# Kernel tuning notes

Measured on AMD Instinct MI355X. Metric: run time of the kernel, lower is better.

## Reference

```python
import jax, jax.numpy as jnp
import numpy as np

B = 65536
IN_DIM = 512
H0, H1 = 256, 128
HEAD_H = 64
D = 12
K_MAX = 3
EPS = 1e-5
# predecessor indices per disease (topologically ordered DAG)
PRED_LISTS = [[], [0], [0], [1, 2], [0, 3], [2], [4, 5], [1, 6], [3, 7], [6, 8], [5, 9], [8, 10, 9]]


def setup_inputs() -> dict:
    key = jax.random.key(0)
    ks = jax.random.split(key, 16)
    x = jax.random.normal(ks[0], (B, IN_DIM), jnp.float32)
    enc_W0 = jax.random.normal(ks[1], (IN_DIM, H0), jnp.float32) * 0.04
    enc_b0 = jnp.zeros((H0,), jnp.float32)
    bn0_g = jnp.ones((H0,), jnp.float32)
    bn0_b = jnp.zeros((H0,), jnp.float32)
    bn0_m = jax.random.normal(ks[2], (H0,), jnp.float32) * 0.1
    bn0_v = jax.random.uniform(ks[3], (H0,), jnp.float32, 0.5, 1.5)
    enc_W1 = jax.random.normal(ks[4], (H0, H1), jnp.float32) * 0.06
    enc_b1 = jnp.zeros((H1,), jnp.float32)
    bn1_g = jnp.ones((H1,), jnp.float32)
    bn1_b = jnp.zeros((H1,), jnp.float32)
    bn1_m = jax.random.normal(ks[5], (H1,), jnp.float32) * 0.1
    bn1_v = jax.random.uniform(ks[6], (H1,), jnp.float32, 0.5, 1.5)
    w_init = jax.random.normal(ks[7], (D, H1), jnp.float32) * 0.09   # head.layer1 (pass-1 logit)
    b_init = jnp.zeros((D,), jnp.float32)
    Wz = jax.random.normal(ks[8], (D, H1, HEAD_H), jnp.float32) * 0.09   # head first layer, z-columns
    Wp = jax.random.normal(ks[9], (D, K_MAX, HEAD_H), jnp.float32) * 0.09  # head first layer, predecessor columns (padded)
    bh = jnp.zeros((D, HEAD_H), jnp.float32)
    Wo = jax.random.normal(ks[10], (D, HEAD_H), jnp.float32) * 0.12
    bo = jnp.zeros((D,), jnp.float32)
    idx = np.zeros((D, K_MAX), np.int32)
    w = np.zeros((D, K_MAX), np.float32)
    for d, preds in enumerate(PRED_LISTS):
        for j, p in enumerate(preds):
            idx[d, j] = p
            w[d, j] = 0.5  # DAG edge weight; zero entries are padding
    return {"x": x, "enc_W0": enc_W0, "enc_b0": enc_b0, "bn0_g": bn0_g, "bn0_b": bn0_b,
            "bn0_m": bn0_m, "bn0_v": bn0_v, "enc_W1": enc_W1, "enc_b1": enc_b1,
            "bn1_g": bn1_g, "bn1_b": bn1_b, "bn1_m": bn1_m, "bn1_v": bn1_v,
            "w_init": w_init, "b_init": b_init, "Wz": Wz, "Wp": Wp, "bh": bh,
            "Wo": Wo, "bo": bo, "pred_w": jnp.asarray(w), "pred_idx": jnp.asarray(idx)}


def reference(x, enc_W0, enc_b0, bn0_g, bn0_b, bn0_m, bn0_v, enc_W1, enc_b1,
              bn1_g, bn1_b, bn1_m, bn1_v, w_init, b_init, Wz, Wp, bh, Wo, bo,
              pred_w, pred_idx):
    # Shared encoder: Linear -> BatchNorm(eval stats) -> ReLU, twice (dropout identity at eval)
    h = x @ enc_W0 + enc_b0
    h = jax.nn.relu((h - bn0_m) * jax.lax.rsqrt(bn0_v + EPS) * bn0_g + bn0_b)
    z = h @ enc_W1 + enc_b1
    z = jax.nn.relu((z - bn1_m) * jax.lax.rsqrt(bn1_v + EPS) * bn1_g + bn1_b)  # [B, H1]
    # Pass 1: initial per-disease prediction = sigmoid(head.layer1(z))
    p = jax.nn.sigmoid(z @ w_init.T + b_init)  # [B, D]
    # Pass 2: DAG gather of predecessor predictions, edge-weighted; padding slots have weight 0
    aug = p[:, pred_idx] * pred_w  # [B, D, K_MAX]
    # Per-disease head: Linear(H1 + k -> HEAD_H) split into z-part + predecessor-part, ReLU, Linear(HEAD_H -> 1), sigmoid
    hid = jax.nn.relu(jnp.einsum('be,deh->bdh', z, Wz) + jnp.einsum('bdk,dkh->bdh', aug, Wp) + bh)
    out = jax.nn.sigmoid(jnp.einsum('bdh,dh->bd', hid, Wo) + bo)  # [B, D] = torch.cat of final_preds
    return out
```

## Files before the change

kernel.cpp:

```cpp
#include <hip/hip_runtime.h>

#define B_TOT   65536
#define IN_DIM  512
#define H0      256
#define H1      128
#define HH      64
#define NDIS    12

typedef __bf16 bf16_t;
typedef __bf16 bf16x4 __attribute__((ext_vector_type(4)));
typedef __bf16 bf16x8 __attribute__((ext_vector_type(8)));
typedef float  f32x4  __attribute__((ext_vector_type(4)));
typedef float  floatx4 __attribute__((ext_vector_type(4)));

#define WS_W0T   0u
#define WS_W1T   262144u
#define WS_WZT   327680u
#define WS_WIT   524288u
#define WS_AL0   528384u
#define WS_BE0   529408u
#define WS_AL1   530432u
#define WS_BE1   530944u
#define WS_NEED  531456u

#define L_XS0    0u
#define L_W0S0   5120u
#define L_XS1    25600u
#define L_W0S1   30720u
#define L_HS     0u
#define L_WZS    0u
#define L_ZS     34816u
#define L_PS     52224u
#define L_WIS    56320u
#define L_TOTAL  60672u

__global__ void prep_kernel(const float* __restrict__ W0, const float* __restrict__ b0,
                            const float* __restrict__ g0, const float* __restrict__ bb0,
                            const float* __restrict__ mm0, const float* __restrict__ vv0,
                            const float* __restrict__ W1, const float* __restrict__ b1,
                            const float* __restrict__ g1, const float* __restrict__ bb1,
                            const float* __restrict__ mm1, const float* __restrict__ vv1,
                            const float* __restrict__ w_init, const float* __restrict__ Wz,
                            char* __restrict__ ws)
{
    bf16_t* W0t = (bf16_t*)(ws + WS_W0T);
    bf16_t* W1t = (bf16_t*)(ws + WS_W1T);
    bf16_t* Wzt = (bf16_t*)(ws + WS_WZT);
    bf16_t* wiT = (bf16_t*)(ws + WS_WIT);
    float* al0 = (float*)(ws + WS_AL0);
    float* be0 = (float*)(ws + WS_BE0);
    float* al1 = (float*)(ws + WS_AL1);
    float* be1 = (float*)(ws + WS_BE1);

    int t = blockIdx.x * 256 + threadIdx.x;

    {
        int c = t >> 9, k = t & 511;
        W0t[t] = (bf16_t)W0[k * H0 + c];
    }
    if (t < H1 * H0) {
        int c = t >> 8, k = t & 255;
        W1t[t] = (bf16_t)W1[k * H1 + c];
    }
    if (t < NDIS * HH * H1) {
        int d = t >> 13, r = t & 8191, h = r >> 7, e = r & 127;
        Wzt[t] = (bf16_t)Wz[d * 8192 + e * 64 + h];
    }
    if (t < 16 * H1) {
        int d = t >> 7, e = t & 127;
        wiT[t] = (d < NDIS) ? (bf16_t)w_init[d * H1 + e] : (bf16_t)0.0f;
    }
    if (t < H0) {
        float a = g0[t] * rsqrtf(vv0[t] + 1e-5f);
        al0[t] = a;
        be0[t] = (b0[t] - mm0[t]) * a + bb0[t];
    }
    if (t < H1) {
        float a = g1[t] * rsqrtf(vv1[t] + 1e-5f);
        al1[t] = a;
        be1[t] = (b1[t] - mm1[t]) * a + bb1[t];
    }
}

__global__ __launch_bounds__(512, 3) void fused_kernel(
    const float* __restrict__ x,
    const bf16_t* __restrict__ W0t, const bf16_t* __restrict__ W1t,
    const float* __restrict__ al0, const float* __restrict__ be0,
    const float* __restrict__ al1, const float* __restrict__ be1,
    const bf16_t* __restrict__ Wzt, const bf16_t* __restrict__ wiT,
    const float* __restrict__ b_init, const float* __restrict__ Wp,
    const float* __restrict__ bh, const float* __restrict__ Wo,
    const float* __restrict__ bo, const float* __restrict__ pred_w,
    const int* __restrict__ pred_idx, float* __restrict__ out)
{
    __shared__ __align__(16) char smem[L_TOTAL];

    const int tid  = threadIdx.x;
    const int lane = tid & 63, wid = tid >> 6;
    const int l15 = lane & 15, lg = lane >> 4;
    const int m0 = blockIdx.x * 64;

    {
        bf16_t* wis = (bf16_t*)(smem + L_WIS);
        if (tid < 256) {
            int row = tid >> 4, k8 = (tid & 15) << 3;
            *(bf16x8*)(wis + row * 136 + k8) = *(const bf16x8*)(wiT + row * H1 + k8);
        }
    }

    const int wr = wid >> 2, wc = wid & 3;
    const int xrow = tid >> 3, xc4 = (tid & 7) << 2;
    const int wrow = tid >> 2, wk8 = (tid & 3) << 3;
    const float*  xp  = x + (m0 + xrow) * IN_DIM + xc4;
    const bf16_t* wp0 = W0t + wrow * IN_DIM + wk8;
    const bf16_t* wp1 = W0t + (wrow + 128) * IN_DIM + wk8;

    bf16_t* xsb[2]  = { (bf16_t*)(smem + L_XS0),  (bf16_t*)(smem + L_XS1)  };
    bf16_t* w0sb[2] = { (bf16_t*)(smem + L_W0S0), (bf16_t*)(smem + L_W0S1) };

    floatx4 xvA, xvB;
    bf16x8  wvA0, wvA1, wvB0, wvB1;

#define LOAD_A(ks) { xvA = *(const floatx4*)(xp + (ks) * 32); \
                     wvA0 = *(const bf16x8*)(wp0 + (ks) * 32); \
                     wvA1 = *(const bf16x8*)(wp1 + (ks) * 32); }
#define LOAD_B(ks) { xvB = *(const floatx4*)(xp + (ks) * 32); \
                     wvB0 = *(const bf16x8*)(wp0 + (ks) * 32); \
                     wvB1 = *(const bf16x8*)(wp1 + (ks) * 32); }
#define STORE_A(bi) { bf16x4 xo; xo[0]=(bf16_t)xvA[0]; xo[1]=(bf16_t)xvA[1]; \
                      xo[2]=(bf16_t)xvA[2]; xo[3]=(bf16_t)xvA[3]; \
                      *(bf16x4*)(xsb[bi] + xrow * 40 + xc4) = xo; \
                      *(bf16x8*)(w0sb[bi] + wrow * 40 + wk8) = wvA0; \
                      *(bf16x8*)(w0sb[bi] + (wrow + 128) * 40 + wk8) = wvA1; }
#define STORE_B(bi) { bf16x4 xo; xo[0]=(bf16_t)xvB[0]; xo[1]=(bf16_t)xvB[1]; \
                      xo[2]=(bf16_t)xvB[2]; xo[3]=(bf16_t)xvB[3]; \
                      *(bf16x4*)(xsb[bi] + xrow * 40 + xc4) = xo; \
                      *(bf16x8*)(w0sb[bi] + wrow * 40 + wk8) = wvB0; \
                      *(bf16x8*)(w0sb[bi] + (wrow + 128) * 40 + wk8) = wvB1; }

    f32x4 acc[2][4] = {};
#define MFMA_STEP(bi) { bf16x8 a[2], b[4]; \
    _Pragma("unroll") \
    for (int mr = 0; mr < 2; ++mr) \
        a[mr] = *(const bf16x8*)(xsb[bi] + (wr * 32 + mr * 16 + l15) * 40 + lg * 8); \
    _Pragma("unroll") \
    for (int nr = 0; nr < 4; ++nr) \
        b[nr] = *(const bf16x8*)(w0sb[bi] + (wc * 64 + nr * 16 + l15) * 40 + lg * 8); \
    _Pragma("unroll") \
    for (int mr = 0; mr < 2; ++mr) \
        _Pragma("unroll") \
        for (int nr = 0; nr < 4; ++nr) \
            acc[mr][nr] = __builtin_amdgcn_mfma_f32_16x16x32_bf16(a[mr], b[nr], acc[mr][nr], 0, 0, 0); }

    LOAD_A(0);
    STORE_A(0);
    LOAD_B(1);
    __syncthreads();

    #pragma unroll
    for (int tt = 0; tt < 8; ++tt) {
        if (tt < 7) LOAD_A(2 * tt + 2);
        MFMA_STEP(0);
        STORE_B(1);
        __syncthreads();
        if (tt < 7) LOAD_B(2 * tt + 3);
        MFMA_STEP(1);
        if (tt < 7) STORE_A(0);
        __syncthreads();
    }

    {
        bf16_t* hs = (bf16_t*)(smem + L_HS);
        #pragma unroll
        for (int mr = 0; mr < 2; ++mr)
            #pragma unroll
            for (int nr = 0; nr < 4; ++nr) {
                int c = wc * 64 + nr * 16 + l15;
                float alpha = al0[c], beta = be0[c];
                #pragma unroll
                for (int j = 0; j < 4; ++j) {
                    int r = wr * 32 + mr * 16 + lg * 4 + j;
                    float v = fmaxf(acc[mr][nr][j] * alpha + beta, 0.0f);
                    hs[r * 264 + c] = (bf16_t)v;
                }
            }
    }
    __syncthreads();

    {
        bf16_t* hs = (bf16_t*)(smem + L_HS);
        bf16_t* zs = (bf16_t*)(smem + L_ZS);
        f32x4 acc2[2][2] = {};
        #pragma unroll
        for (int kf = 0; kf < 8; ++kf) {
            bf16x8 a[2], b[2];
            #pragma unroll
            for (int mr = 0; mr < 2; ++mr)
                a[mr] = *(const bf16x8*)(hs + (wr * 32 + mr * 16 + l15) * 264 + kf * 32 + lg * 8);
            #pragma unroll
            for (int nr = 0; nr < 2; ++nr) {
                int c = wc * 32 + nr * 16 + l15;
                b[nr] = *(const bf16x8*)(W1t + c * H0 + kf * 32 + lg * 8);
            }
            #pragma unroll
            for (int mr = 0; mr < 2; ++mr)
                #pragma unroll
                for (int nr = 0; nr < 2; ++nr)
                    acc2[mr][nr] = __builtin_amdgcn_mfma_f32_16x16x32_bf16(a[mr], b[nr], acc2[mr][nr], 0, 0, 0);
        }
        #pragma unroll
        for (int mr = 0; mr < 2; ++mr)
            #pragma unroll
            for (int nr = 0; nr < 2; ++nr) {
                int c = wc * 32 + nr * 16 + l15;
                float alpha = al1[c], beta = be1[c];
                #pragma unroll
                for (int j = 0; j < 4; ++j) {
                    int r = wr * 32 + mr * 16 + lg * 4 + j;
                    float v = fmaxf(acc2[mr][nr][j] * alpha + beta, 0.0f);
                    zs[r * 136 + c] = (bf16_t)v;
                }
            }
    }
    __syncthreads();

    {
        bf16_t* zs  = (bf16_t*)(smem + L_ZS);
        bf16_t* wis = (bf16_t*)(smem + L_WIS);
        float*  ps  = (float*)(smem + L_PS);
        if (wid < 4) {
            f32x4 pacc = {};
            #pragma unroll
            for (int kf = 0; kf < 4; ++kf) {
                bf16x8 a = *(const bf16x8*)(zs + (wid * 16 + l15) * 136 + kf * 32 + lg * 8);
                bf16x8 b = *(const bf16x8*)(wis + l15 * 136 + kf * 32 + lg * 8);
                pacc = __builtin_amdgcn_mfma_f32_16x16x32_bf16(a, b, pacc, 0, 0, 0);
            }
            int d = l15;
            float bi = (d < NDIS) ? b_init[d] : 0.0f;
            #pragma unroll
            for (int j = 0; j < 4; ++j) {
                int r = wid * 16 + lg * 4 + j;
                ps[r * 16 + d] = 1.0f / (1.0f + __expf(-(pacc[j] + bi)));
            }
        }
    }
    __syncthreads();

    {
        bf16_t* zs  = (bf16_t*)(smem + L_ZS);
        float*  ps  = (float*)(smem + L_PS);
        const int g  = wid >> 2;
        const int mt = wid & 3;
        const int lt = tid & 255;
        bf16_t* wzs = (bf16_t*)(smem + L_WZS) + g * 8704;

        for (int i = 0; i < 6; ++i) {
            int d = g * 6 + i;
            #pragma unroll
            for (int j = 0; j < 4; ++j) {
                int chunk = j * 256 + lt;
                int row = chunk >> 4, k8 = (chunk & 15) << 3;
                *(bf16x8*)(wzs + row * 136 + k8) = *(const bf16x8*)(Wzt + d * 8192 + row * H1 + k8);
            }
            __syncthreads();

            f32x4 hacc[4] = {};
            #pragma unroll
            for (int kf = 0; kf < 4; ++kf) {
                bf16x8 a = *(const bf16x8*)(zs + (mt * 16 + l15) * 136 + kf * 32 + lg * 8);
                #pragma unroll
                for (int nr = 0; nr < 4; ++nr) {
                    bf16x8 b = *(const bf16x8*)(wzs + (nr * 16 + l15) * 136 + kf * 32 + lg * 8);
                    hacc[nr] = __builtin_amdgcn_mfma_f32_16x16x32_bf16(a, b, hacc[nr], 0, 0, 0);
                }
            }

            int i0 = pred_idx[d * 3 + 0], i1 = pred_idx[d * 3 + 1], i2 = pred_idx[d * 3 + 2];
            float w0p = pred_w[d * 3 + 0], w1p = pred_w[d * 3 + 1], w2p = pred_w[d * 3 + 2];
            float bod = bo[d];

            float aug0[4], aug1[4], aug2[4];
            #pragma unroll
            for (int j = 0; j < 4; ++j) {
                int r = mt * 16 + lg * 4 + j;
                aug0[j] = ps[r * 16 + i0] * w0p;
                aug1[j] = ps[r * 16 + i1] * w1p;
                aug2[j] = ps[r * 16 + i2] * w2p;
            }
            float res[4] = {0.f, 0.f, 0.f, 0.f};
            #pragma unroll
            for (int nr = 0; nr < 4; ++nr) {
                int c = nr * 16 + l15;
                float bhv = bh[d * 64 + c];
                float wpa = Wp[d * 192 + c], wpb = Wp[d * 192 + 64 + c], wpc = Wp[d * 192 + 128 + c];
                float wov = Wo[d * 64 + c];
                #pragma unroll
                for (int j = 0; j < 4; ++j) {
                    float v = hacc[nr][j] + bhv + aug0[j] * wpa + aug1[j] * wpb + aug2[j] * wpc;
                    res[j] += fmaxf(v, 0.0f) * wov;
                }
            }
            #pragma unroll
            for (int j = 0; j < 4; ++j) {
                float s = res[j];
                s += __shfl_xor(s, 1); s += __shfl_xor(s, 2);
                s += __shfl_xor(s, 4); s += __shfl_xor(s, 8);
                if (l15 == 0) {
                    int r = mt * 16 + lg * 4 + j;
                    out[(m0 + r) * NDIS + d] = 1.0f / (1.0f + __expf(-(s + bod)));
                }
            }
            __syncthreads();
        }
    }
}

extern "C" void kernel_launch(void* const* d_in, const int* in_sizes, int n_in,
                              void* d_out, int out_size, void* d_ws, size_t ws_size,
                              hipStream_t stream) {
    if (ws_size < (size_t)WS_NEED) return;

    const float* x      = (const float*)d_in[0];
    const float* W0     = (const float*)d_in[1];
    const float* b0     = (const float*)d_in[2];
    const float* g0     = (const float*)d_in[3];
    const float* bb0    = (const float*)d_in[4];
    const float* mm0    = (const float*)d_in[5];
    const float* vv0    = (const float*)d_in[6];
    const float* W1     = (const float*)d_in[7];
    const float* b1     = (const float*)d_in[8];
    const float* g1     = (const float*)d_in[9];
    const float* bb1    = (const float*)d_in[10];
    const float* vv1_   = (const float*)d_in[12];
    const float* mm1    = (const float*)d_in[11];
    const float* w_init = (const float*)d_in[13];
    const float* b_init = (const float*)d_in[14];
    const float* Wz     = (const float*)d_in[15];
    const float* Wp     = (const float*)d_in[16];
    const float* bh     = (const float*)d_in[17];
    const float* Wo     = (const float*)d_in[18];
    const float* bo     = (const float*)d_in[19];
    const float* pred_w = (const float*)d_in[20];
    const int*   pred_idx = (const int*)d_in[21];

    char* ws = (char*)d_ws;
    const bf16_t* W0t = (const bf16_t*)(ws + WS_W0T);
    const bf16_t* W1t = (const bf16_t*)(ws + WS_W1T);
    const bf16_t* Wzt = (const bf16_t*)(ws + WS_WZT);
    const bf16_t* wiT = (const bf16_t*)(ws + WS_WIT);
    const float* al0 = (const float*)(ws + WS_AL0);
    const float* be0 = (const float*)(ws + WS_BE0);
    const float* al1 = (const float*)(ws + WS_AL1);
    const float* be1 = (const float*)(ws + WS_BE1);

    prep_kernel<<<dim3(512), dim3(256), 0, stream>>>(
        W0, b0, g0, bb0, mm0, vv0, W1, b1, g1, bb1, mm1, vv1_, w_init, Wz, ws);

    fused_kernel<<<dim3(B_TOT / 64), dim3(512), 0, stream>>>(
        x, W0t, W1t, al0, be0, al1, be1, Wzt, wiT, b_init, Wp, bh, Wo, bo,
        pred_w, pred_idx, (float*)d_out);
}
```

Baseline: 91.33 us.

## Read weights directly from global/L2 and stage only x in shared memory

The first GEMM no longer stages W0 tiles through LDS. Only x is double-buffered, in larger 128-wide K chunks with fewer barriers, and the B fragments are read straight from the bf16 W0t in global memory. The per-disease head also reads Wz and w_init directly from global instead of copying them to LDS, which removes the per-disease syncthreads. The freed LDS shrinks the block footprint so occupancy can go from 3 to 4 blocks per CU, and the ps stride is padded to 17. The trade is more redundant global/L2 traffic for the weight fragments in exchange for fewer LDS writes and barriers.

Measured after the change: 191.2 us. 2.09x slower.

```diff
diff --git a/kernel.cpp b/kernel.cpp
--- a/kernel.cpp
+++ b/kernel.cpp
@@ -24,15 +24,11 @@
 #define WS_NEED  531456u
 
 #define L_XS0    0u
-#define L_W0S0   5120u
-#define L_XS1    25600u
-#define L_W0S1   30720u
+#define L_XS1    17408u
 #define L_HS     0u
-#define L_WZS    0u
+#define L_PS     0u
 #define L_ZS     34816u
-#define L_PS     52224u
-#define L_WIS    56320u
-#define L_TOTAL  60672u
+#define L_TOTAL  52224u
 
 __global__ void prep_kernel(const float* __restrict__ W0, const float* __restrict__ b0,
                             const float* __restrict__ g0, const float* __restrict__ bb0,
@@ -82,7 +78,7 @@
     }
 }
 
-__global__ __launch_bounds__(512, 3) void fused_kernel(
+__global__ __launch_bounds__(512, 4) void fused_kernel(
     const float* __restrict__ x,
     const bf16_t* __restrict__ W0t, const bf16_t* __restrict__ W1t,
     const float* __restrict__ al0, const float* __restrict__ be0,
@@ -100,72 +96,50 @@
     const int l15 = lane & 15, lg = lane >> 4;
     const int m0 = blockIdx.x * 64;
 
-    {
-        bf16_t* wis = (bf16_t*)(smem + L_WIS);
-        if (tid < 256) {
-            int row = tid >> 4, k8 = (tid & 15) << 3;
-            *(bf16x8*)(wis + row * 136 + k8) = *(const bf16x8*)(wiT + row * H1 + k8);
+    bf16_t* xsb[2] = { (bf16_t*)(smem + L_XS0), (bf16_t*)(smem + L_XS1) };
+
+    const int wr = wid >> 2, wc = wid & 3;
+    const int xrow0 = tid >> 5;
+    const int xc    = (tid & 31) << 2;
+    const float* xg = x + (m0 + xrow0) * IN_DIM + xc;
+
+#define XLOAD(v, ks) { _Pragma("unroll") \
+    for (int i = 0; i < 4; ++i) v[i] = *(const floatx4*)(xg + i * 16 * IN_DIM + (ks) * 128); }
+#define XSTORE(v, bi) { _Pragma("unroll") \
+    for (int i = 0; i < 4; ++i) { bf16x4 o; \
+        o[0] = (bf16_t)v[i][0]; o[1] = (bf16_t)v[i][1]; \
+        o[2] = (bf16_t)v[i][2]; o[3] = (bf16_t)v[i][3]; \
+        *(bf16x4*)(xsb[bi] + (xrow0 + 16 * i) * 136 + xc) = o; } }
+
+    f32x4 acc[2][4] = {};
+
+    {
+        floatx4 v[4];
+        XLOAD(v, 0);
+        XSTORE(v, 0);
+    }
+    __syncthreads();
+
+    #pragma unroll
+    for (int ks = 0; ks < 4; ++ks) {
+        floatx4 v[4];
+        if (ks < 3) XLOAD(v, ks + 1);
+        #pragma unroll
+        for (int kf = 0; kf < 4; ++kf) {
+            bf16x8 a[2], b[4];
+            #pragma unroll
+            for (int mr = 0; mr < 2; ++mr)
+                a[mr] = *(const bf16x8*)(xsb[ks & 1] + (wr * 32 + mr * 16 + l15) * 136 + kf * 32 + lg * 8);
+            #pragma unroll
+            for (int nr = 0; nr < 4; ++nr)
+                b[nr] = *(const bf16x8*)(W0t + (wc * 64 + nr * 16 + l15) * IN_DIM + ks * 128 + kf * 32 + lg * 8);
+            #pragma unroll
+            for (int mr = 0; mr < 2; ++mr)
+                #pragma unroll
+                for (int nr = 0; nr < 4; ++nr)
+                    acc[mr][nr] = __builtin_amdgcn_mfma_f32_16x16x32_bf16(a[mr], b[nr], acc[mr][nr], 0, 0, 0);
         }
-    }
-
-    const int wr = wid >> 2, wc = wid & 3;
-    const int xrow = tid >> 3, xc4 = (tid & 7) << 2;
-    const int wrow = tid >> 2, wk8 = (tid & 3) << 3;
-    const float*  xp  = x + (m0 + xrow) * IN_DIM + xc4;
-    const bf16_t* wp0 = W0t + wrow * IN_DIM + wk8;
-    const bf16_t* wp1 = W0t + (wrow + 128) * IN_DIM + wk8;
-
-    bf16_t* xsb[2]  = { (bf16_t*)(smem + L_XS0),  (bf16_t*)(smem + L_XS1)  };
-    bf16_t* w0sb[2] = { (bf16_t*)(smem + L_W0S0), (bf16_t*)(smem + L_W0S1) };
-
-    floatx4 xvA, xvB;
-    bf16x8  wvA0, wvA1, wvB0, wvB1;
-
-#define LOAD_A(ks) { xvA = *(const floatx4*)(xp + (ks) * 32); \
-                     wvA0 = *(const bf16x8*)(wp0 + (ks) * 32); \
-                     wvA1 = *(const bf16x8*)(wp1 + (ks) * 32); }
-#define LOAD_B(ks) { xvB = *(const floatx4*)(xp + (ks) * 32); \
-                     wvB0 = *(const bf16x8*)(wp0 + (ks) * 32); \
-                     wvB1 = *(const bf16x8*)(wp1 + (ks) * 32); }
-#define STORE_A(bi) { bf16x4 xo; xo[0]=(bf16_t)xvA[0]; xo[1]=(bf16_t)xvA[1]; \
-                      xo[2]=(bf16_t)xvA[2]; xo[3]=(bf16_t)xvA[3]; \
-                      *(bf16x4*)(xsb[bi] + xrow * 40 + xc4) = xo; \
-                      *(bf16x8*)(w0sb[bi] + wrow * 40 + wk8) = wvA0; \
-                      *(bf16x8*)(w0sb[bi] + (wrow + 128) * 40 + wk8) = wvA1; }
-#define STORE_B(bi) { bf16x4 xo; xo[0]=(bf16_t)xvB[0]; xo[1]=(bf16_t)xvB[1]; \
-                      xo[2]=(bf16_t)xvB[2]; xo[3]=(bf16_t)xvB[3]; \
-                      *(bf16x4*)(xsb[bi] + xrow * 40 + xc4) = xo; \
-                      *(bf16x8*)(w0sb[bi] + wrow * 40 + wk8) = wvB0; \
-                      *(bf16x8*)(w0sb[bi] + (wrow + 128) * 40 + wk8) = wvB1; }
-
-    f32x4 acc[2][4] = {};
-#define MFMA_STEP(bi) { bf16x8 a[2], b[4]; \
-    _Pragma("unroll") \
-    for (int mr = 0; mr < 2; ++mr) \
-        a[mr] = *(const bf16x8*)(xsb[bi] + (wr * 32 + mr * 16 + l15) * 40 + lg * 8); \
-    _Pragma("unroll") \
-    for (int nr = 0; nr < 4; ++nr) \
-        b[nr] = *(const bf16x8*)(w0sb[bi] + (wc * 64 + nr * 16 + l15) * 40 + lg * 8); \
-    _Pragma("unroll") \
-    for (int mr = 0; mr < 2; ++mr) \
-        _Pragma("unroll") \
-        for (int nr = 0; nr < 4; ++nr) \
-            acc[mr][nr] = __builtin_amdgcn_mfma_f32_16x16x32_bf16(a[mr], b[nr], acc[mr][nr], 0, 0, 0); }
-
-    LOAD_A(0);
-    STORE_A(0);
-    LOAD_B(1);
-    __syncthreads();
-
-    #pragma unroll
-    for (int tt = 0; tt < 8; ++tt) {
-        if (tt < 7) LOAD_A(2 * tt + 2);
-        MFMA_STEP(0);
-        STORE_B(1);
-        __syncthreads();
-        if (tt < 7) LOAD_B(2 * tt + 3);
-        MFMA_STEP(1);
-        if (tt < 7) STORE_A(0);
+        if (ks < 3) XSTORE(v, (ks + 1) & 1);
         __syncthreads();
     }
 
@@ -198,10 +172,8 @@
             for (int mr = 0; mr < 2; ++mr)
                 a[mr] = *(const bf16x8*)(hs + (wr * 32 + mr * 16 + l15) * 264 + kf * 32 + lg * 8);
             #pragma unroll
-            for (int nr = 0; nr < 2; ++nr) {
-                int c = wc * 32 + nr * 16 + l15;
-                b[nr] = *(const bf16x8*)(W1t + c * H0 + kf * 32 + lg * 8);
-            }
+            for (int nr = 0; nr < 2; ++nr)
+                b[nr] = *(const bf16x8*)(W1t + (wc * 32 + nr * 16 + l15) * H0 + kf * 32 + lg * 8);
             #pragma unroll
             for (int mr = 0; mr < 2; ++mr)
                 #pragma unroll
@@ -225,15 +197,14 @@
     __syncthreads();
 
     {
-        bf16_t* zs  = (bf16_t*)(smem + L_ZS);
-        bf16_t* wis = (bf16_t*)(smem + L_WIS);
-        float*  ps  = (float*)(smem + L_PS);
+        bf16_t* zs = (bf16_t*)(smem + L_ZS);
+        float*  ps = (float*)(smem + L_PS);
         if (wid < 4) {
             f32x4 pacc = {};
             #pragma unroll
             for (int kf = 0; kf < 4; ++kf) {
                 bf16x8 a = *(const bf16x8*)(zs + (wid * 16 + l15) * 136 + kf * 32 + lg * 8);
-                bf16x8 b = *(const bf16x8*)(wis + l15 * 136 + kf * 32 + lg * 8);
+                bf16x8 b = *(const bf16x8*)(wiT + l15 * H1 + kf * 32 + lg * 8);
                 pacc = __builtin_amdgcn_mfma_f32_16x16x32_bf16(a, b, pacc, 0, 0, 0);
             }
             int d = l15;
@@ -241,29 +212,20 @@
             #pragma unroll
             for (int j = 0; j < 4; ++j) {
                 int r = wid * 16 + lg * 4 + j;
-                ps[r * 16 + d] = 1.0f / (1.0f + __expf(-(pacc[j] + bi)));
+                ps[r * 17 + d] = 1.0f / (1.0f + __expf(-(pacc[j] + bi)));
             }
         }
     }
     __syncthreads();
 
     {
-        bf16_t* zs  = (bf16_t*)(smem + L_ZS);
-        float*  ps  = (float*)(smem + L_PS);
+        bf16_t* zs = (bf16_t*)(smem + L_ZS);
+        float*  ps = (float*)(smem + L_PS);
         const int g  = wid >> 2;
         const int mt = wid & 3;
-        const int lt = tid & 255;
-        bf16_t* wzs = (bf16_t*)(smem + L_WZS) + g * 8704;
 
         for (int i = 0; i < 6; ++i) {
             int d = g * 6 + i;
-            #pragma unroll
-            for (int j = 0; j < 4; ++j) {
-                int chunk = j * 256 + lt;
-                int row = chunk >> 4, k8 = (chunk & 15) << 3;
-                *(bf16x8*)(wzs + row * 136 + k8) = *(const bf16x8*)(Wzt + d * 8192 + row * H1 + k8);
-            }
-            __syncthreads();
 
             f32x4 hacc[4] = {};
             #pragma unroll
@@ -271,7 +233,7 @@
                 bf16x8 a = *(const bf16x8*)(zs + (mt * 16 + l15) * 136 + kf * 32 + lg * 8);
                 #pragma unroll
                 for (int nr = 0; nr < 4; ++nr) {
-                    bf16x8 b = *(const bf16x8*)(wzs + (nr * 16 + l15) * 136 + kf * 32 + lg * 8);
+                    bf16x8 b = *(const bf16x8*)(Wzt + d * 8192 + (nr * 16 + l15) * H1 + kf * 32 + lg * 8);
                     hacc[nr] = __builtin_amdgcn_mfma_f32_16x16x32_bf16(a, b, hacc[nr], 0, 0, 0);
                 }
             }
@@ -284,9 +246,9 @@
             #pragma unroll
             for (int j = 0; j < 4; ++j) {
                 int r = mt * 16 + lg * 4 + j;
-                aug0[j] = ps[r * 16 + i0] * w0p;
-                aug1[j] = ps[r * 16 + i1] * w1p;
-                aug2[j] = ps[r * 16 + i2] * w2p;
+                aug0[j] = ps[r * 17 + i0] * w0p;
+                aug1[j] = ps[r * 17 + i1] * w1p;
+                aug2[j] = ps[r * 17 + i2] * w2p;
             }
             float res[4] = {0.f, 0.f, 0.f, 0.f};
             #pragma unroll
@@ -311,7 +273,6 @@
                     out[(m0 + r) * NDIS + d] = 1.0f / (1.0f + __expf(-(s + bod)));
                 }
             }
-            __syncthreads();
         }
     }
 }
@@ -332,8 +293,8 @@
     const float* b1     = (const float*)d_in[8];
     const float* g1     = (const float*)d_in[9];
     const float* bb1    = (const float*)d_in[10];
-    const float* vv1_   = (const float*)d_in[12];
     const float* mm1    = (const float*)d_in[11];
+    const float* vv1    = (const float*)d_in[12];
     const float* w_init = (const float*)d_in[13];
     const float* b_init = (const float*)d_in[14];
     const float* Wz     = (const float*)d_in[15];
@@ -355,7 +316,7 @@
     const float* be1 = (const float*)(ws + WS_BE1);
 
     prep_kernel<<<dim3(512), dim3(256), 0, stream>>>(
-        W0, b0, g0, bb0, mm0, vv0, W1, b1, g1, bb1, mm1, vv1_, w_init, Wz, ws);
+        W0, b0, g0, bb0, mm0, vv0, W1, b1, g1, bb1, mm1, vv1, w_init, Wz, ws);
 
     fused_kernel<<<dim3(B_TOT / 64), dim3(512), 0, stream>>>(
         x, W0t, W1t, al0, be0, al1, be1, Wzt, wiT, b_init, Wp, bh, Wo, bo,
```
